# Kernel tuning notes

Measured on AMD Instinct MI355X. Metric: run time of the kernel, lower is better.

Reference implementation:

```python
import jax, jax.numpy as jnp
import numpy as np

N, E, F, H, L, G, C, NC = 100000, 1200000, 32, 64, 3, 256, 200000, 10
D = L * H  # concat node embedding dim = 192


def setup_inputs() -> dict:
    key = jax.random.key(0)
    ks = jax.random.split(key, 20)

    def w(k, shape):
        fan_in = shape[-2] if len(shape) > 1 else shape[0]
        return jax.random.normal(k, shape, jnp.float32) * (1.0 / np.sqrt(fan_in))

    inp = dict(
        x=jax.random.normal(ks[0], (N, F), jnp.float32),
        edge_index=jax.random.randint(ks[1], (2, E), 0, N),
        batch=jnp.sort(jax.random.randint(ks[2], (N,), 0, G)),
        cand_node=jax.random.randint(ks[3], (C,), 0, N),
        c1_W1=w(ks[4], (F, H)), c1_b1=jnp.zeros((H,)),
        c1_W2=w(ks[5], (H, H)), c1_b2=jnp.zeros((H,)),
        c1_g=jnp.ones((H,)), c1_be=jnp.zeros((H,)), c1_m=jnp.zeros((H,)), c1_v=jnp.ones((H,)),
        c1_eps=jnp.zeros((1,)),
        cs_W1=w(ks[6], (L - 1, H, H)), cs_b1=jnp.zeros((L - 1, H)),
        cs_W2=w(ks[7], (L - 1, H, H)), cs_b2=jnp.zeros((L - 1, H)),
        cs_g=jnp.ones((L - 1, H)), cs_be=jnp.zeros((L - 1, H)),
        cs_m=jnp.zeros((L - 1, H)), cs_v=jnp.ones((L - 1, H)),
        cs_eps=jnp.zeros((L - 1,)),
        nc_W1=w(ks[8], (D, 2 * H)), nc_b1=jnp.zeros((2 * H,)),
        nc_W2=w(ks[9], (2 * H, H)), nc_b2=jnp.zeros((H,)),
        nc_W3=w(ks[10], (H, H)), nc_b3=jnp.zeros((H,)),
        nc_W4=w(ks[11], (H, NC)), nc_b4=jnp.zeros((NC,)),
        comp_emb=jax.random.normal(ks[12], (NC, D), jnp.float32),
        ep_W1=w(ks[13], (2 * D, 2 * H)), ep_b1=jnp.zeros((2 * H,)),
        ep_W2=w(ks[14], (2 * H, H)), ep_b2=jnp.zeros((H,)),
        ep_W3=w(ks[15], (H, 1)), ep_b3=jnp.zeros((1,)),
    )
    return inp


def _bn(h, g, b, m, v):
    # BatchNorm1d in eval mode with running stats
    return g * (h - m) * jax.lax.rsqrt(v + 1e-5) + b


def _gin_layer(h, src, dst, eps, W1, b1, W2, b2, g, be, m, v):
    agg = jax.ops.segment_sum(h[src], dst, num_segments=N)  # sum aggregation
    h = (1.0 + eps) * h + agg
    h = jax.nn.relu(h @ W1 + b1)
    h = jax.nn.relu(h @ W2 + b2)
    return _bn(h, g, be, m, v)


def reference(x, edge_index, batch, cand_node,
              c1_W1, c1_b1, c1_W2, c1_b2, c1_g, c1_be, c1_m, c1_v, c1_eps,
              cs_W1, cs_b1, cs_W2, cs_b2, cs_g, cs_be, cs_m, cs_v, cs_eps,
              nc_W1, nc_b1, nc_W2, nc_b2, nc_W3, nc_b3, nc_W4, nc_b4,
              comp_emb, ep_W1, ep_b1, ep_W2, ep_b2, ep_W3, ep_b3):
    src, dst = edge_index[0], edge_index[1]
    # shared GIN encoder: concat per-layer node embeddings -> [N, L*H]
    h = _gin_layer(x, src, dst, c1_eps, c1_W1, c1_b1, c1_W2, c1_b2, c1_g, c1_be, c1_m, c1_v)
    xs = [h]
    for i in range(cs_W1.shape[0]):
        h = _gin_layer(h, src, dst, cs_eps[i], cs_W1[i], cs_b1[i], cs_W2[i], cs_b2[i],
                       cs_g[i], cs_be[i], cs_m[i], cs_v[i])
        xs.append(h)
    node_emb = jnp.concatenate(xs, axis=-1)  # [N, D]

    # global mean pool per graph -> classification head (dropout=identity in eval)
    sums = jax.ops.segment_sum(node_emb, batch, num_segments=G)
    cnt = jax.ops.segment_sum(jnp.ones((node_emb.shape[0], 1), node_emb.dtype), batch, num_segments=G)
    graph_emb = sums / jnp.maximum(cnt, 1.0)  # [G, D]
    hc = jax.nn.relu(graph_emb @ nc_W1 + nc_b1)
    hc = jax.nn.relu(hc @ nc_W2 + nc_b2)
    hc = jax.nn.relu(hc @ nc_W3 + nc_b3)
    logits = hc @ nc_W4 + nc_b4
    class_output = jax.nn.log_softmax(logits, axis=-1)  # [G, NC]

    # link prediction: predicted comp type per graph, score all candidates in one batch
    comp_idx = jnp.argmax(class_output, axis=-1)          # [G]
    cand_graph = batch[cand_node]                          # [C]
    ce = comp_emb[comp_idx[cand_graph]]                    # [C, D]
    de = node_emb[cand_node]                               # [C, D]
    ef = jnp.concatenate([ce, de], axis=-1)                # [C, 2D]
    he = jax.nn.relu(ef @ ep_W1 + ep_b1)
    he = jax.nn.relu(he @ ep_W2 + ep_b2)
    edge_scores = jax.nn.sigmoid((he @ ep_W3 + ep_b3).squeeze(-1))  # [C]
    return class_output, edge_scores
```

## Files before the change

kernel.cpp:

```cpp
#include <hip/hip_runtime.h>
#include <hip/hip_bf16.h>


#define GG 256
#define NCC 10
#define DD 192
#define BSH 9

typedef short bf16x8 __attribute__((ext_vector_type(8)));
typedef float f32x4  __attribute__((ext_vector_type(4)));

__device__ inline unsigned short f2bf_u(float x) {
    __hip_bfloat16 h = __float2bfloat16(x);
    return *reinterpret_cast<unsigned short*>(&h);
}
__device__ inline float bf2f(unsigned short u) {
    return __uint_as_float(((unsigned int)u) << 16);
}

__global__ void bin_hist(const int* __restrict__ dst, int* __restrict__ bcnt, int E_) {
    __shared__ int h[256];
    h[threadIdx.x] = 0;
    __syncthreads();
    for (int e = blockIdx.x * 256 + threadIdx.x; e < E_; e += gridDim.x * 256)
        atomicAdd(&h[dst[e] >> BSH], 1);
    __syncthreads();
    if (h[threadIdx.x]) atomicAdd(&bcnt[threadIdx.x], h[threadIdx.x]);
}

__global__ void bin_scan(const int* __restrict__ bcnt, int* __restrict__ bbase,
                         int* __restrict__ bpos, int NB, int E_) {
    __shared__ int s[256];
    const int t = threadIdx.x;
    int v = (t < NB) ? bcnt[t] : 0;
    s[t] = v;
    __syncthreads();
    for (int off = 1; off < 256; off <<= 1) {
        int x = (t >= off) ? s[t - off] : 0;
        __syncthreads();
        s[t] += x;
        __syncthreads();
    }
    if (t < NB) { bbase[t] = s[t] - v; bpos[t] = s[t] - v; }
    if (t == 0) bbase[NB] = E_;
}

__global__ __launch_bounds__(256) void bin_scatter(
    const int* __restrict__ src, const int* __restrict__ dst,
    int* __restrict__ bpos, int2* __restrict__ ebuf, int E_) {
    __shared__ int h[256];
    __shared__ int base[256];
    const int t = threadIdx.x;
    const int e0 = blockIdx.x * 2048;
    h[t] = 0;
    __syncthreads();
    int myb[8], mys[8], myd[8], myr[8];
    #pragma unroll
    for (int u = 0; u < 8; ++u) {
        int e = e0 + t + u * 256;
        if (e < E_) {
            int d = dst[e];
            myb[u] = d >> BSH;
            myd[u] = d;
            mys[u] = src[e];
            myr[u] = atomicAdd(&h[myb[u]], 1);
        } else myb[u] = -1;
    }
    __syncthreads();
    if (h[t]) base[t] = atomicAdd(&bpos[t], h[t]);
    __syncthreads();
    #pragma unroll
    for (int u = 0; u < 8; ++u)
        if (myb[u] >= 0)
            ebuf[base[myb[u]] + myr[u]] = make_int2(mys[u], myd[u]);
}

__global__ __launch_bounds__(256) void csr_bucket(
    const int2* __restrict__ ebuf, const int* __restrict__ bbase,
    int* __restrict__ rowptr, int* __restrict__ nbr, int N_, int NB) {
    __shared__ int lh[512];
    __shared__ int lx[512];
    __shared__ int ps[256];
    const int b = blockIdx.x;
    const int t = threadIdx.x;
    const int ebase = bbase[b], eend = bbase[b + 1];
    const int ecnt = eend - ebase;
    const int n0 = b << BSH;

    for (int i = t; i < 512; i += 256) lh[i] = 0;
    __syncthreads();
    for (int i = t; i < ecnt; i += 256)
        atomicAdd(&lh[ebuf[ebase + i].y - n0], 1);
    __syncthreads();

    int pv = lh[2 * t] + lh[2 * t + 1];
    ps[t] = pv;
    __syncthreads();
    for (int off = 1; off < 256; off <<= 1) {
        int x = (t >= off) ? ps[t - off] : 0;
        __syncthreads();
        ps[t] += x;
        __syncthreads();
    }
    const int excl = ps[t] - pv;
    lx[2 * t] = excl;
    lx[2 * t + 1] = excl + lh[2 * t];
    __syncthreads();

    for (int i = t; i < 512; i += 256) {
        int n = n0 + i;
        if (n < N_) rowptr[n] = ebase + lx[i];
    }
    if (b == NB - 1 && t == 0) rowptr[N_] = eend;

    for (int i = t; i < 512; i += 256) lh[i] = lx[i];
    __syncthreads();
    for (int i = t; i < ecnt; i += 256) {
        int2 p = ebuf[ebase + i];
        int r = atomicAdd(&lh[p.y - n0], 1);
        nbr[ebase + r] = p.x;
    }
}

__global__ void prep_enc(const float* __restrict__ c1W1, const float* __restrict__ c1W2,
                         const float* __restrict__ csW1, const float* __restrict__ csW2,
                         unsigned short* __restrict__ enc) {
    int idx = blockIdx.x * 256 + threadIdx.x;
    if (idx >= 22528) return;
    const float* W; int rel;
    if (idx < 2048)       { W = c1W1;        rel = idx; }
    else if (idx < 6144)  { W = c1W2;        rel = idx - 2048; }
    else if (idx < 10240) { W = csW1;        rel = idx - 6144; }
    else if (idx < 14336) { W = csW2;        rel = idx - 10240; }
    else if (idx < 18432) { W = csW1 + 4096; rel = idx - 14336; }
    else                  { W = csW2 + 4096; rel = idx - 18432; }
    int frag = rel >> 9;
    int lane = (rel >> 3) & 63;
    int j = rel & 7;
    int ks = frag >> 2, nt = frag & 3;
    int k = ks * 32 + ((lane >> 4) << 3) + j;
    int n = nt * 16 + (lane & 15);
    enc[idx] = f2bf_u(W[k * 64 + n]);
}

__global__ void gcnt_bs(const int* __restrict__ batch, int* __restrict__ gcnt_i, int N_) {
    __shared__ int lbs[GG + 1];
    const int g = threadIdx.x;
    int lo = 0, hi = N_;
    while (lo < hi) {
        int mid = (lo + hi) >> 1;
        if (batch[mid] < g) lo = mid + 1; else hi = mid;
    }
    lbs[g] = lo;
    if (g == 0) lbs[GG] = N_;
    __syncthreads();
    gcnt_i[g] = lbs[g + 1] - lbs[g];
}

#define SWZ(row, byte) ((byte) ^ (((row) & 7) << 4))

template<int K>
__global__ __launch_bounds__(512) void gin_fused(
    const float* __restrict__ x32,
    const __hip_bfloat16* __restrict__ hin_b,
    const int* __restrict__ rowptr, const int* __restrict__ nbr,
    const unsigned short* __restrict__ W1p, const float* __restrict__ b1,
    const unsigned short* __restrict__ W2p, const float* __restrict__ b2,
    const float* __restrict__ gamma, const float* __restrict__ beta,
    const float* __restrict__ mean, const float* __restrict__ var,
    const float* __restrict__ eps_p,
    __hip_bfloat16* __restrict__ out_b,
    const int* __restrict__ batch, float* __restrict__ gsum, int soff,
    int N_) {
    __shared__ char s_agg[32 * 128];
    __shared__ char s_h1[32 * 128];
    __shared__ char s_out[32 * 128];
    __shared__ int sb[32];

    const int t = threadIdx.x;
    const int lane = t & 63;
    const int w = t >> 6;
    const int node0 = blockIdx.x * 32;
    const int nb = w * 4;

    if (t < 32) sb[t] = (node0 + t < N_) ? batch[node0 + t] : -1;

    const float eps1 = 1.0f + eps_p[0];

    const int n0w = node0 + nb;
    const int rp0 = __builtin_amdgcn_readfirstlane(rowptr[min(n0w + 0, N_)]);
    const int rp1 = __builtin_amdgcn_readfirstlane(rowptr[min(n0w + 1, N_)]);
    const int rp2 = __builtin_amdgcn_readfirstlane(rowptr[min(n0w + 2, N_)]);
    const int rp3 = __builtin_amdgcn_readfirstlane(rowptr[min(n0w + 3, N_)]);
    const int rp4 = __builtin_amdgcn_readfirstlane(rowptr[min(n0w + 4, N_)]);
    const int cnt = rp4 - rp0;
    const int e1 = rp1 - rp0, e2 = rp2 - rp0, e3 = rp3 - rp0;
    const int* nbp = nbr + rp0;

    float a0 = 0.f, a1 = 0.f, a2 = 0.f, a3 = 0.f;

    if (K == 64) {
        const __hip_bfloat16* hbp = hin_b + lane;
        int idxb[16];
        #pragma unroll
        for (int u = 0; u < 16; ++u) idxb[u] = nbp[u];
        for (int k = 0; k < cnt; k += 16) {
            int nxt[16];
            #pragma unroll
            for (int u = 0; u < 16; ++u) nxt[u] = nbp[k + 16 + u];
            #pragma unroll
            for (int u = 0; u < 16; ++u) {
                float v = __bfloat162float(hbp[(size_t)idxb[u] * DD]);
                int j = k + u;
                a0 += (j < e1)             ? v : 0.f;
                a1 += (j >= e1 && j < e2)  ? v : 0.f;
                a2 += (j >= e2 && j < e3)  ? v : 0.f;
                a3 += (j >= e3 && j < cnt) ? v : 0.f;
            }
            #pragma unroll
            for (int u = 0; u < 16; ++u) idxb[u] = nxt[u];
        }
        if (n0w + 0 < N_) a0 += eps1 * __bfloat162float(hbp[(size_t)(n0w + 0) * DD]);
        if (n0w + 1 < N_) a1 += eps1 * __bfloat162float(hbp[(size_t)(n0w + 1) * DD]);
        if (n0w + 2 < N_) a2 += eps1 * __bfloat162float(hbp[(size_t)(n0w + 2) * DD]);
        if (n0w + 3 < N_) a3 += eps1 * __bfloat162float(hbp[(size_t)(n0w + 3) * DD]);
        *(unsigned short*)(s_agg + SWZ(nb + 0, (nb + 0) * 128 + lane * 2)) = f2bf_u(a0);
        *(unsigned short*)(s_agg + SWZ(nb + 1, (nb + 1) * 128 + lane * 2)) = f2bf_u(a1);
        *(unsigned short*)(s_agg + SWZ(nb + 2, (nb + 2) * 128 + lane * 2)) = f2bf_u(a2);
        *(unsigned short*)(s_agg + SWZ(nb + 3, (nb + 3) * 128 + lane * 2)) = f2bf_u(a3);
    } else {
        const int d = lane & 31, rs = lane >> 5;
        const float* xp = x32 + d;
        int idxb[8];
        #pragma unroll
        for (int u = 0; u < 8; ++u) idxb[u] = nbp[2 * u + rs];
        for (int k = 0; k < cnt; k += 16) {
            int nxt[8];
            #pragma unroll
            for (int u = 0; u < 8; ++u) nxt[u] = nbp[k + 16 + 2 * u + rs];
            #pragma unroll
            for (int u = 0; u < 8; ++u) {
                float v = xp[(size_t)idxb[u] * 32];
                int j = k + 2 * u + rs;
                a0 += (j < e1)             ? v : 0.f;
                a1 += (j >= e1 && j < e2)  ? v : 0.f;
                a2 += (j >= e2 && j < e3)  ? v : 0.f;
                a3 += (j >= e3 && j < cnt) ? v : 0.f;
            }
            #pragma unroll
            for (int u = 0; u < 8; ++u) idxb[u] = nxt[u];
        }
        a0 += __shfl_xor(a0, 32);
        a1 += __shfl_xor(a1, 32);
        a2 += __shfl_xor(a2, 32);
        a3 += __shfl_xor(a3, 32);
        if (rs == 0) {
            if (n0w + 0 < N_) a0 += eps1 * xp[(size_t)(n0w + 0) * 32];
            if (n0w + 1 < N_) a1 += eps1 * xp[(size_t)(n0w + 1) * 32];
            if (n0w + 2 < N_) a2 += eps1 * xp[(size_t)(n0w + 2) * 32];
            if (n0w + 3 < N_) a3 += eps1 * xp[(size_t)(n0w + 3) * 32];
            *(unsigned short*)(s_agg + SWZ(nb + 0, (nb + 0) * 128 + d * 2)) = f2bf_u(a0);
            *(unsigned short*)(s_agg + SWZ(nb + 1, (nb + 1) * 128 + d * 2)) = f2bf_u(a1);
            *(unsigned short*)(s_agg + SWZ(nb + 2, (nb + 2) * 128 + d * 2)) = f2bf_u(a2);
            *(unsigned short*)(s_agg + SWZ(nb + 3, (nb + 3) * 128 + d * 2)) = f2bf_u(a3);
        }
    }
    __syncthreads();

    const int mt = w >> 2, nt = w & 3;
    const int arow = mt * 16 + (lane & 15);
    const int col = nt * 16 + (lane & 15);
    f32x4 c1v = (f32x4){0.f, 0.f, 0.f, 0.f};
    #pragma unroll
    for (int ks = 0; ks < K / 32; ++ks) {
        bf16x8 a = *(const bf16x8*)(s_agg + SWZ(arow, arow * 128 + ks * 64 + ((lane >> 4) << 4)));
        bf16x8 b = *(const bf16x8*)(W1p + (((ks << 2) + nt) << 9) + (lane << 3));
        c1v = __builtin_amdgcn_mfma_f32_16x16x32_bf16(a, b, c1v, 0, 0, 0);
    }
    {
        const float bb1 = b1[col];
        #pragma unroll
        for (int reg = 0; reg < 4; ++reg) {
            int row = mt * 16 + ((lane >> 4) << 2) + reg;
            float v = fmaxf(c1v[reg] + bb1, 0.f);
            *(unsigned short*)(s_h1 + SWZ(row, row * 128 + col * 2)) = f2bf_u(v);
        }
    }
    __syncthreads();

    f32x4 c2v = (f32x4){0.f, 0.f, 0.f, 0.f};
    #pragma unroll
    for (int ks = 0; ks < 2; ++ks) {
        bf16x8 a = *(const bf16x8*)(s_h1 + SWZ(arow, arow * 128 + ks * 64 + ((lane >> 4) << 4)));
        bf16x8 b = *(const bf16x8*)(W2p + (((ks << 2) + nt) << 9) + (lane << 3));
        c2v = __builtin_amdgcn_mfma_f32_16x16x32_bf16(a, b, c2v, 0, 0, 0);
    }
    {
        const float bb2 = b2[col];
        const float ga = gamma[col], bet = beta[col], mu = mean[col];
        const float iv = rsqrtf(var[col] + 1e-5f);
        #pragma unroll
        for (int reg = 0; reg < 4; ++reg) {
            int row = mt * 16 + ((lane >> 4) << 2) + reg;
            float v = fmaxf(c2v[reg] + bb2, 0.f);
            v = ga * (v - mu) * iv + bet;
            *(unsigned short*)(s_out + SWZ(row, row * 128 + col * 2)) = f2bf_u(v);
        }
    }
    __syncthreads();

    {
        int r = t >> 4, c8 = t & 15;
        int node = node0 + r;
        if (node < N_) {
            ushort4 v = *(const ushort4*)(s_out + SWZ(r, r * 128 + c8 * 8));
            *(ushort4*)((unsigned short*)out_b + (size_t)node * DD + c8 * 4) = v;
        }
    }

    if (t < 256) {
        const int d = t & 63;
        const int rg = t >> 6;
        float acc = 0.f;
        int curg = sb[rg * 8];
        #pragma unroll
        for (int r = rg * 8; r < rg * 8 + 8; ++r) {
            int g = sb[r];
            if (g != curg) {
                if (curg >= 0) atomicAdd(&gsum[curg * DD + soff + d], acc);
                acc = 0.f; curg = g;
            }
            if (g >= 0)
                acc += bf2f(*(const unsigned short*)(s_out + SWZ(r, r * 128 + d * 2)));
        }
        if (curg >= 0) atomicAdd(&gsum[curg * DD + soff + d], acc);
    }
}

__global__ void head_kernel(const float* __restrict__ gsum, const int* __restrict__ gcnt_i,
                            const float* __restrict__ W1, const float* __restrict__ b1,
                            const float* __restrict__ W2, const float* __restrict__ b2,
                            const float* __restrict__ W3, const float* __restrict__ b3,
                            const float* __restrict__ W4, const float* __restrict__ b4,
                            float* __restrict__ class_out, int* __restrict__ comp_idx) {
    const int g = blockIdx.x;
    const int t = threadIdx.x;
    __shared__ float ge[DD], h1[128], h2[64], h3[64], logits[NCC];

    const float c = fmaxf((float)gcnt_i[g], 1.0f);
    if (t < DD) ge[t] = gsum[g * DD + t] / c;
    __syncthreads();

    if (t < 128) {
        float a = b1[t];
        #pragma unroll 4
        for (int k = 0; k < DD; ++k) a += ge[k] * W1[k * 128 + t];
        h1[t] = fmaxf(a, 0.0f);
    }
    __syncthreads();
    if (t < 64) {
        float a = b2[t];
        #pragma unroll 4
        for (int k = 0; k < 128; ++k) a += h1[k] * W2[k * 64 + t];
        h2[t] = fmaxf(a, 0.0f);
    }
    __syncthreads();
    if (t < 64) {
        float a = b3[t];
        #pragma unroll 4
        for (int k = 0; k < 64; ++k) a += h2[k] * W3[k * 64 + t];
        h3[t] = fmaxf(a, 0.0f);
    }
    __syncthreads();
    if (t < NCC) {
        float a = b4[t];
        #pragma unroll
        for (int k = 0; k < 64; ++k) a += h3[k] * W4[k * NCC + t];
        logits[t] = a;
    }
    __syncthreads();
    if (t == 0) {
        float mx = logits[0]; int am = 0;
        for (int j = 1; j < NCC; ++j) if (logits[j] > mx) { mx = logits[j]; am = j; }
        float se = 0.0f;
        for (int j = 0; j < NCC; ++j) se += expf(logits[j] - mx);
        float lse = logf(se);
        for (int j = 0; j < NCC; ++j) class_out[g * NCC + j] = logits[j] - mx - lse;
        comp_idx[g] = am;
    }
}

__global__ void prep_edge(const float* __restrict__ W1, const float* __restrict__ b1,
                          const float* __restrict__ W2, const float* __restrict__ comp_emb,
                          unsigned short* __restrict__ W1b_p, unsigned short* __restrict__ W2_p,
                          float* __restrict__ pc) {
    int idx = blockIdx.x * 256 + threadIdx.x;
    const int S1 = 6 * 8 * 512;
    const int S2 = 4 * 4 * 512;
    if (idx < S1) {
        int frag = idx >> 9;
        int lane = (idx >> 3) & 63;
        int j = idx & 7;
        int kstep = frag >> 3, nt = frag & 7;
        int k = kstep * 32 + ((lane >> 4) << 3) + j;
        int n = nt * 16 + (lane & 15);
        W1b_p[idx] = f2bf_u(W1[(192 + k) * 128 + n]);
    } else if (idx < S1 + S2) {
        int i2 = idx - S1;
        int frag = i2 >> 9;
        int lane = (i2 >> 3) & 63;
        int j = i2 & 7;
        int kstep = frag >> 2, nt = frag & 3;
        int k = kstep * 32 + ((lane >> 4) << 3) + j;
        int n = nt * 16 + (lane & 15);
        W2_p[i2] = f2bf_u(W2[k * 64 + n]);
    } else if (idx < S1 + S2 + NCC * 128) {
        int i3 = idx - (S1 + S2);
        int ci = i3 >> 7, col = i3 & 127;
        float a = b1[col];
        for (int k = 0; k < DD; ++k) a += comp_emb[ci * DD + k] * W1[k * 128 + col];
        pc[i3] = a;
    }
}

__global__ __launch_bounds__(256, 5) void edge_mfma(
    const int* __restrict__ cand, const int* __restrict__ batch,
    const int* __restrict__ comp_idx, const short* __restrict__ hb,
    const unsigned short* __restrict__ W1b_p, const unsigned short* __restrict__ W2_p,
    const float* __restrict__ pc, const float* __restrict__ W3,
    const float* __restrict__ b3, float* __restrict__ scores, int C_) {
    __shared__ char s_buf[64 * 384];
    __shared__ float s_part[4][64];
    __shared__ int s_node[64];
    __shared__ int s_ci[64];
    __shared__ float s_w3[64];

    const int t = threadIdx.x;
    const int lane = t & 63;
    const int w = t >> 6;
    const int c0 = blockIdx.x * 64;

    if (t < 64) {
        int c = c0 + t;
        int node = (c < C_) ? cand[c] : cand[0];
        s_node[t] = node;
        s_ci[t] = comp_idx[batch[node]];
        s_w3[t] = W3[t];
    }
    __syncthreads();

    for (int i = t; i < 64 * 24; i += 256) {
        int r = i / 24, c8 = i - r * 24;
        bf16x8 v = *(const bf16x8*)(hb + (size_t)s_node[r] * DD + c8 * 8);
        *(bf16x8*)(s_buf + SWZ(r, r * 384 + c8 * 16)) = v;
    }
    __syncthreads();

    f32x4 acc1[4][2];
    #pragma unroll
    for (int rt = 0; rt < 4; ++rt)
        #pragma unroll
        for (int b = 0; b < 2; ++b) acc1[rt][b] = (f32x4){0.f, 0.f, 0.f, 0.f};
    #pragma unroll
    for (int ks = 0; ks < 6; ++ks) {
        bf16x8 b0 = *(const bf16x8*)(W1b_p + ((ks * 8 + 2 * w + 0) << 9) + (lane << 3));
        bf16x8 b1f = *(const bf16x8*)(W1b_p + ((ks * 8 + 2 * w + 1) << 9) + (lane << 3));
        #pragma unroll
        for (int rt = 0; rt < 4; ++rt) {
            int arow = rt * 16 + (lane & 15);
            bf16x8 a = *(const bf16x8*)(s_buf + SWZ(arow, arow * 384 + ks * 64 + ((lane >> 4) << 4)));
            acc1[rt][0] = __builtin_amdgcn_mfma_f32_16x16x32_bf16(a, b0, acc1[rt][0], 0, 0, 0);
            acc1[rt][1] = __builtin_amdgcn_mfma_f32_16x16x32_bf16(a, b1f, acc1[rt][1], 0, 0, 0);
        }
    }
    __syncthreads();

    #pragma unroll
    for (int rt = 0; rt < 4; ++rt) {
        #pragma unroll
        for (int reg = 0; reg < 4; ++reg) {
            int row = rt * 16 + ((lane >> 4) << 2) + reg;
            int ci = s_ci[row];
            #pragma unroll
            for (int b = 0; b < 2; ++b) {
                int col = (2 * w + b) * 16 + (lane & 15);
                float v = fmaxf(acc1[rt][b][reg] + pc[ci * 128 + col], 0.f);
                *(unsigned short*)(s_buf + SWZ(row, row * 256 + col * 2)) = f2bf_u(v);
            }
        }
    }
    __syncthreads();

    f32x4 acc2[4];
    #pragma unroll
    for (int rt = 0; rt < 4; ++rt) acc2[rt] = (f32x4){0.f, 0.f, 0.f, 0.f};
    #pragma unroll
    for (int ks = 0; ks < 4; ++ks) {
        bf16x8 b = *(const bf16x8*)(W2_p + ((ks * 4 + w) << 9) + (lane << 3));
        #pragma unroll
        for (int rt = 0; rt < 4; ++rt) {
            int arow = rt * 16 + (lane & 15);
            bf16x8 a = *(const bf16x8*)(s_buf + SWZ(arow, arow * 256 + ks * 64 + ((lane >> 4) << 4)));
            acc2[rt] = __builtin_amdgcn_mfma_f32_16x16x32_bf16(a, b, acc2[rt], 0, 0, 0);
        }
    }

    {
        const float w3v = s_w3[w * 16 + (lane & 15)];
        #pragma unroll
        for (int rt = 0; rt < 4; ++rt) {
            #pragma unroll
            for (int reg = 0; reg < 4; ++reg) {
                float p = fmaxf(acc2[rt][reg], 0.f) * w3v;
                p += __shfl_xor(p, 1);
                p += __shfl_xor(p, 2);
                p += __shfl_xor(p, 4);
                p += __shfl_xor(p, 8);
                if ((lane & 15) == 0)
                    s_part[w][rt * 16 + ((lane >> 4) << 2) + reg] = p;
            }
        }
    }
    __syncthreads();

    if (t < 64) {
        int c = c0 + t;
        if (c < C_) {
            float p = s_part[0][t] + s_part[1][t] + s_part[2][t] + s_part[3][t] + b3[0];
            scores[c] = 1.0f / (1.0f + expf(-p));
        }
    }
}

extern "C" void kernel_launch(void* const* d_in, const int* in_sizes, int n_in,
                              void* d_out, int out_size, void* d_ws, size_t ws_size,
                              hipStream_t stream) {
    const float* x        = (const float*)d_in[0];
    const int*   ei       = (const int*)d_in[1];
    const int*   batch    = (const int*)d_in[2];
    const int*   cand     = (const int*)d_in[3];
    const float* c1_W1    = (const float*)d_in[4];
    const float* c1_b1    = (const float*)d_in[5];
    const float* c1_W2    = (const float*)d_in[6];
    const float* c1_b2    = (const float*)d_in[7];
    const float* c1_g     = (const float*)d_in[8];
    const float* c1_be    = (const float*)d_in[9];
    const float* c1_m     = (const float*)d_in[10];
    const float* c1_v     = (const float*)d_in[11];
    const float* c1_eps   = (const float*)d_in[12];
    const float* cs_W1    = (const float*)d_in[13];
    const float* cs_b1    = (const float*)d_in[14];
    const float* cs_W2    = (const float*)d_in[15];
    const float* cs_b2    = (const float*)d_in[16];
    const float* cs_g     = (const float*)d_in[17];
    const float* cs_be    = (const float*)d_in[18];
    const float* cs_m     = (const float*)d_in[19];
    const float* cs_v     = (const float*)d_in[20];
    const float* cs_eps   = (const float*)d_in[21];
    const float* nc_W1    = (const float*)d_in[22];
    const float* nc_b1    = (const float*)d_in[23];
    const float* nc_W2    = (const float*)d_in[24];
    const float* nc_b2    = (const float*)d_in[25];
    const float* nc_W3    = (const float*)d_in[26];
    const float* nc_b3    = (const float*)d_in[27];
    const float* nc_W4    = (const float*)d_in[28];
    const float* nc_b4    = (const float*)d_in[29];
    const float* comp_emb = (const float*)d_in[30];
    const float* ep_W1    = (const float*)d_in[31];
    const float* ep_b1    = (const float*)d_in[32];
    const float* ep_W2    = (const float*)d_in[33];
    const float* ep_b2    = (const float*)d_in[34];
    const float* ep_W3    = (const float*)d_in[35];
    const float* ep_b3    = (const float*)d_in[36];

    const int N_ = in_sizes[0] / 32;
    const int E_ = in_sizes[1] / 2;
    const int C_ = in_sizes[3];
    const int* src = ei;
    const int* dst = ei + E_;
    const int NB = (N_ + (1 << BSH) - 1) >> BSH;

    char* ws = (char*)d_ws;
    size_t off = 0;
    __hip_bfloat16* hb = (__hip_bfloat16*)(ws + off); off += (size_t)N_ * DD * 2;
    int*   rowptr   = (int*)(ws + off);   off += (size_t)(N_ + 2) * 4;
    int*   nbr      = (int*)(ws + off);   off += (size_t)(E_ + 64) * 4;
    int*   bcnt     = (int*)(ws + off);   off += 1024;
    int*   bbase    = (int*)(ws + off);   off += 1044;
    int*   bpos     = (int*)(ws + off);   off += 1024;
    float* gsum     = (float*)(ws + off); off += (size_t)GG * DD * 4;
    int*   gcnt_i   = (int*)(ws + off);   off += 1024;
    int*   comp_idx = (int*)(ws + off);   off += 1024;
    float* pc       = (float*)(ws + off); off += NCC * 128 * 4;
    unsigned short* W1b_p = (unsigned short*)(ws + off); off += 6 * 8 * 512 * 2;
    unsigned short* W2_p  = (unsigned short*)(ws + off); off += 4 * 4 * 512 * 2;
    unsigned short* enc   = (unsigned short*)(ws + off); off += 22528 * 2;
    int2*  ebuf     = (int2*)hb;

    float* class_out = (float*)d_out;
    float* scores    = class_out + GG * NCC;

    prep_edge<<<(6 * 8 * 512 + 4 * 4 * 512 + NCC * 128 + 255) / 256, 256, 0, stream>>>(
        ep_W1, ep_b1, ep_W2, comp_emb, W1b_p, W2_p, pc);
    prep_enc<<<(22528 + 255) / 256, 256, 0, stream>>>(c1_W1, c1_W2, cs_W1, cs_W2, enc);

    hipMemsetAsync(bcnt, 0, 1024, stream);
    hipMemsetAsync(nbr + E_, 0, 64 * 4, stream);
    bin_hist<<<1024, 256, 0, stream>>>(dst, bcnt, E_);
    bin_scan<<<1, 256, 0, stream>>>(bcnt, bbase, bpos, NB, E_);
    bin_scatter<<<(E_ + 2047) / 2048, 256, 0, stream>>>(src, dst, bpos, ebuf, E_);
    csr_bucket<<<NB, 256, 0, stream>>>(ebuf, bbase, rowptr, nbr, N_, NB);

    hipMemsetAsync(gsum, 0, (size_t)GG * DD * 4, stream);
    gcnt_bs<<<1, GG, 0, stream>>>(batch, gcnt_i, N_);

    const int gblk = (N_ + 31) / 32;
    gin_fused<32><<<gblk, 512, 0, stream>>>(
        x, nullptr, rowptr, nbr,
        enc + 0, c1_b1, enc + 2048, c1_b2,
        c1_g, c1_be, c1_m, c1_v, c1_eps, hb + 0, batch, gsum, 0, N_);
    gin_fused<64><<<gblk, 512, 0, stream>>>(
        nullptr, hb + 0, rowptr, nbr,
        enc + 6144, cs_b1 + 0, enc + 10240, cs_b2 + 0,
        cs_g + 0, cs_be + 0, cs_m + 0, cs_v + 0, cs_eps + 0, hb + 64, batch, gsum, 64, N_);
    gin_fused<64><<<gblk, 512, 0, stream>>>(
        nullptr, hb + 64, rowptr, nbr,
        enc + 14336, cs_b1 + 64, enc + 18432, cs_b2 + 64,
        cs_g + 64, cs_be + 64, cs_m + 64, cs_v + 64, cs_eps + 1, hb + 128, batch, gsum, 128, N_);

    head_kernel<<<GG, 256, 0, stream>>>(gsum, gcnt_i, nc_W1, nc_b1, nc_W2, nc_b2,
                                        nc_W3, nc_b3, nc_W4, nc_b4, class_out, comp_idx);

    edge_mfma<<<(C_ + 63) / 64, 256, 0, stream>>>(
        cand, batch, comp_idx, (const short*)hb, W1b_p, W2_p, pc, ep_W3, ep_b3, scores, C_);
}
```

Baseline: 296.6 us.

## Convert x to bf16 and pipeline gathers with prefix-sum segmented accumulation

Adds a pre-pass that converts the fp32 input features to bf16 so the first GIN layer gathers half as many bytes per neighbor. The 64-wide layers now double-buffer neighbor gathers across two register arrays and accumulate a single running sum, recovering the four per-node sums from prefix differences only when a segment boundary falls inside the current chunk. This cuts per-element select/add work and keeps more loads in flight. The cost is an extra conversion kernel and buffer, more registers, and slight rounding differences from bf16 x and from subtracting prefix sums.

```diff
diff --git a/kernel.cpp b/kernel.cpp
--- a/kernel.cpp
+++ b/kernel.cpp
@@ -119,6 +119,18 @@
         int2 p = ebuf[ebase + i];
         int r = atomicAdd(&lh[p.y - n0], 1);
         nbr[ebase + r] = p.x;
+    }
+}
+
+__global__ void x2b_kernel(const float* __restrict__ x, unsigned short* __restrict__ xb,
+                           int n_elem) {
+    int i = blockIdx.x * 256 + threadIdx.x;
+    int stride = gridDim.x * 256;
+    for (; i * 4 < n_elem; i += stride) {
+        float4 v = *(const float4*)(x + i * 4);
+        ushort4 u;
+        u.x = f2bf_u(v.x); u.y = f2bf_u(v.y); u.z = f2bf_u(v.z); u.w = f2bf_u(v.w);
+        *(ushort4*)(xb + i * 4) = u;
     }
 }
 
@@ -159,10 +171,39 @@
 
 #define SWZ(row, byte) ((byte) ^ (((row) & 7) << 4))
 
+#define GSTEP(VCUR, VNXT)                                                     \
+    _Pragma("unroll")                                                         \
+    for (int u = 0; u < 16; ++u)                                              \
+        VNXT[u] = bf2f(*(const unsigned short*)(hbase + (unsigned)idx[u] * (unsigned)(DD*2) + lane2)); \
+    _Pragma("unroll")                                                         \
+    for (int u = 0; u < 16; ++u) idx[u] = nbp[k + 32 + u];                    \
+    {                                                                         \
+        float runk = run;                                                     \
+        _Pragma("unroll")                                                     \
+        for (int u = 0; u < 16; ++u) run += VCUR[u];                          \
+        if ((unsigned)(e1 - k) < 16u) { float tt = runk;                      \
+            _Pragma("unroll")                                                 \
+            for (int u = 0; u < 16; ++u) tt += (u < e1 - k) ? VCUR[u] : 0.f;  \
+            s0 = tt; }                                                        \
+        if ((unsigned)(e2 - k) < 16u) { float tt = runk;                      \
+            _Pragma("unroll")                                                 \
+            for (int u = 0; u < 16; ++u) tt += (u < e2 - k) ? VCUR[u] : 0.f;  \
+            s1 = tt; }                                                        \
+        if ((unsigned)(e3 - k) < 16u) { float tt = runk;                      \
+            _Pragma("unroll")                                                 \
+            for (int u = 0; u < 16; ++u) tt += (u < e3 - k) ? VCUR[u] : 0.f;  \
+            s2 = tt; }                                                        \
+        if ((unsigned)(cnt - k) < 16u) { float tt = runk;                     \
+            _Pragma("unroll")                                                 \
+            for (int u = 0; u < 16; ++u) tt += (u < cnt - k) ? VCUR[u] : 0.f; \
+            s3 = tt; }                                                        \
+    }                                                                         \
+    k += 16;                                                                  \
+    if (k > cnt) break;
+
 template<int K>
 __global__ __launch_bounds__(512) void gin_fused(
-    const float* __restrict__ x32,
-    const __hip_bfloat16* __restrict__ hin_b,
+    const unsigned short* __restrict__ hin_b,
     const int* __restrict__ rowptr, const int* __restrict__ nbr,
     const unsigned short* __restrict__ W1p, const float* __restrict__ b1,
     const unsigned short* __restrict__ W2p, const float* __restrict__ b2,
@@ -200,37 +241,35 @@
     float a0 = 0.f, a1 = 0.f, a2 = 0.f, a3 = 0.f;
 
     if (K == 64) {
-        const __hip_bfloat16* hbp = hin_b + lane;
-        int idxb[16];
-        #pragma unroll
-        for (int u = 0; u < 16; ++u) idxb[u] = nbp[u];
-        for (int k = 0; k < cnt; k += 16) {
-            int nxt[16];
-            #pragma unroll
-            for (int u = 0; u < 16; ++u) nxt[u] = nbp[k + 16 + u];
-            #pragma unroll
-            for (int u = 0; u < 16; ++u) {
-                float v = __bfloat162float(hbp[(size_t)idxb[u] * DD]);
-                int j = k + u;
-                a0 += (j < e1)             ? v : 0.f;
-                a1 += (j >= e1 && j < e2)  ? v : 0.f;
-                a2 += (j >= e2 && j < e3)  ? v : 0.f;
-                a3 += (j >= e3 && j < cnt) ? v : 0.f;
-            }
-            #pragma unroll
-            for (int u = 0; u < 16; ++u) idxb[u] = nxt[u];
-        }
-        if (n0w + 0 < N_) a0 += eps1 * __bfloat162float(hbp[(size_t)(n0w + 0) * DD]);
-        if (n0w + 1 < N_) a1 += eps1 * __bfloat162float(hbp[(size_t)(n0w + 1) * DD]);
-        if (n0w + 2 < N_) a2 += eps1 * __bfloat162float(hbp[(size_t)(n0w + 2) * DD]);
-        if (n0w + 3 < N_) a3 += eps1 * __bfloat162float(hbp[(size_t)(n0w + 3) * DD]);
+        const char* hbase = (const char*)hin_b;
+        const unsigned lane2 = (unsigned)lane * 2u;
+        int idx[16];
+        float vA[16], vB[16];
+        float run = 0.f, s0 = 0.f, s1 = 0.f, s2 = 0.f, s3 = 0.f;
+        #pragma unroll
+        for (int u = 0; u < 16; ++u) idx[u] = nbp[u];
+        #pragma unroll
+        for (int u = 0; u < 16; ++u)
+            vA[u] = bf2f(*(const unsigned short*)(hbase + (unsigned)idx[u] * (unsigned)(DD*2) + lane2));
+        #pragma unroll
+        for (int u = 0; u < 16; ++u) idx[u] = nbp[16 + u];
+        for (int k = 0;;) {
+            GSTEP(vA, vB)
+            GSTEP(vB, vA)
+        }
+        a0 = s0; a1 = s1 - s0; a2 = s2 - s1; a3 = s3 - s2;
+        const unsigned short* hbp = hin_b + lane;
+        if (n0w + 0 < N_) a0 += eps1 * bf2f(hbp[(size_t)(n0w + 0) * DD]);
+        if (n0w + 1 < N_) a1 += eps1 * bf2f(hbp[(size_t)(n0w + 1) * DD]);
+        if (n0w + 2 < N_) a2 += eps1 * bf2f(hbp[(size_t)(n0w + 2) * DD]);
+        if (n0w + 3 < N_) a3 += eps1 * bf2f(hbp[(size_t)(n0w + 3) * DD]);
         *(unsigned short*)(s_agg + SWZ(nb + 0, (nb + 0) * 128 + lane * 2)) = f2bf_u(a0);
         *(unsigned short*)(s_agg + SWZ(nb + 1, (nb + 1) * 128 + lane * 2)) = f2bf_u(a1);
         *(unsigned short*)(s_agg + SWZ(nb + 2, (nb + 2) * 128 + lane * 2)) = f2bf_u(a2);
         *(unsigned short*)(s_agg + SWZ(nb + 3, (nb + 3) * 128 + lane * 2)) = f2bf_u(a3);
     } else {
         const int d = lane & 31, rs = lane >> 5;
-        const float* xp = x32 + d;
+        const unsigned short* xp = hin_b + d;
         int idxb[8];
         #pragma unroll
         for (int u = 0; u < 8; ++u) idxb[u] = nbp[2 * u + rs];
@@ -240,7 +279,7 @@
             for (int u = 0; u < 8; ++u) nxt[u] = nbp[k + 16 + 2 * u + rs];
             #pragma unroll
             for (int u = 0; u < 8; ++u) {
-                float v = xp[(size_t)idxb[u] * 32];
+                float v = bf2f(xp[(size_t)idxb[u] * 32]);
                 int j = k + 2 * u + rs;
                 a0 += (j < e1)             ? v : 0.f;
                 a1 += (j >= e1 && j < e2)  ? v : 0.f;
@@ -255,10 +294,10 @@
         a2 += __shfl_xor(a2, 32);
         a3 += __shfl_xor(a3, 32);
         if (rs == 0) {
-            if (n0w + 0 < N_) a0 += eps1 * xp[(size_t)(n0w + 0) * 32];
-            if (n0w + 1 < N_) a1 += eps1 * xp[(size_t)(n0w + 1) * 32];
-            if (n0w + 2 < N_) a2 += eps1 * xp[(size_t)(n0w + 2) * 32];
-            if (n0w + 3 < N_) a3 += eps1 * xp[(size_t)(n0w + 3) * 32];
+            if (n0w + 0 < N_) a0 += eps1 * bf2f(xp[(size_t)(n0w + 0) * 32]);
+            if (n0w + 1 < N_) a1 += eps1 * bf2f(xp[(size_t)(n0w + 1) * 32]);
+            if (n0w + 2 < N_) a2 += eps1 * bf2f(xp[(size_t)(n0w + 2) * 32]);
+            if (n0w + 3 < N_) a3 += eps1 * bf2f(xp[(size_t)(n0w + 3) * 32]);
             *(unsigned short*)(s_agg + SWZ(nb + 0, (nb + 0) * 128 + d * 2)) = f2bf_u(a0);
             *(unsigned short*)(s_agg + SWZ(nb + 1, (nb + 1) * 128 + d * 2)) = f2bf_u(a1);
             *(unsigned short*)(s_agg + SWZ(nb + 2, (nb + 2) * 128 + d * 2)) = f2bf_u(a2);
@@ -583,6 +622,7 @@
     char* ws = (char*)d_ws;
     size_t off = 0;
     __hip_bfloat16* hb = (__hip_bfloat16*)(ws + off); off += (size_t)N_ * DD * 2;
+    unsigned short* xb = (unsigned short*)(ws + off); off += (size_t)N_ * 32 * 2;
     int*   rowptr   = (int*)(ws + off);   off += (size_t)(N_ + 2) * 4;
     int*   nbr      = (int*)(ws + off);   off += (size_t)(E_ + 64) * 4;
     int*   bcnt     = (int*)(ws + off);   off += 1024;
@@ -603,6 +643,7 @@
     prep_edge<<<(6 * 8 * 512 + 4 * 4 * 512 + NCC * 128 + 255) / 256, 256, 0, stream>>>(
         ep_W1, ep_b1, ep_W2, comp_emb, W1b_p, W2_p, pc);
     prep_enc<<<(22528 + 255) / 256, 256, 0, stream>>>(c1_W1, c1_W2, cs_W1, cs_W2, enc);
+    x2b_kernel<<<2048, 256, 0, stream>>>(x, xb, N_ * 32);
 
     hipMemsetAsync(bcnt, 0, 1024, stream);
     hipMemsetAsync(nbr + E_, 0, 64 * 4, stream);
@@ -616,15 +657,15 @@
 
     const int gblk = (N_ + 31) / 32;
     gin_fused<32><<<gblk, 512, 0, stream>>>(
-        x, nullptr, rowptr, nbr,
+        xb, rowptr, nbr,
         enc + 0, c1_b1, enc + 2048, c1_b2,
         c1_g, c1_be, c1_m, c1_v, c1_eps, hb + 0, batch, gsum, 0, N_);
     gin_fused<64><<<gblk, 512, 0, stream>>>(
-        nullptr, hb + 0, rowptr, nbr,
+        (const unsigned short*)hb + 0, rowptr, nbr,
         enc + 6144, cs_b1 + 0, enc + 10240, cs_b2 + 0,
         cs_g + 0, cs_be + 0, cs_m + 0, cs_v + 0, cs_eps + 0, hb + 64, batch, gsum, 64, N_);
     gin_fused<64><<<gblk, 512, 0, stream>>>(
-        nullptr, hb + 64, rowptr, nbr,
+        (const unsigned short*)hb + 64, rowptr, nbr,
         enc + 14336, cs_b1 + 64, enc + 18432, cs_b2 + 64,
         cs_g + 64, cs_be + 64, cs_m + 64, cs_v + 64, cs_eps + 1, hb + 128, batch, gsum, 128, N_);
 
```

New measurement: 300.4 us. No clear change (+1.3%).
